# Kernel tuning notes

Measured on AMD Instinct MI355X. Metric: run time of the kernel, lower is better.

The kernel has to match this reference:

```python
import jax, jax.numpy as jnp
import numpy as np

EMB = 64
HID = 1024
SEQ = 9
BATCH = 4096


def setup_inputs() -> dict:
    key = jax.random.key(0)
    ks = jax.random.split(key, 10)
    s = lambda *sh: 1.0 / np.sqrt(sh[-1])
    return {
        "observed": jax.random.normal(ks[0], (SEQ, BATCH, 2), dtype=jnp.float32),
        "W_emb": jax.random.normal(ks[1], (EMB, 2), dtype=jnp.float32) * s(2),
        "b_emb": jnp.zeros((EMB,), dtype=jnp.float32),
        "W_ih": jax.random.normal(ks[2], (4 * HID, EMB), dtype=jnp.float32) * s(EMB),
        "b_ih": jnp.zeros((4 * HID,), dtype=jnp.float32),
        "W_hh": jax.random.normal(ks[3], (4 * HID, HID), dtype=jnp.float32) * s(HID),
        "b_hh": jnp.zeros((4 * HID,), dtype=jnp.float32),
        "W_out": jax.random.normal(ks[4], (5, HID), dtype=jnp.float32) * s(HID),
        "b_out": jnp.zeros((5,), dtype=jnp.float32),
        "n_predict": 12,
    }


def _cell(x, h, c, W_ih, b_ih, W_hh, b_hh):
    # torch.nn.LSTMCell gate math, gate order i, f, g, o
    gates = x @ W_ih.T + b_ih + h @ W_hh.T + b_hh  # [B, 4H]
    i, f, g, o = jnp.split(gates, 4, axis=-1)
    c_new = jax.nn.sigmoid(f) * c + jax.nn.sigmoid(i) * jnp.tanh(g)
    h_new = jax.nn.sigmoid(o) * jnp.tanh(c_new)
    return h_new, c_new


def reference(observed, W_emb, b_emb, W_ih, b_ih, W_hh, b_hh, W_out, b_out, n_predict):
    B = observed.shape[1]
    H = W_hh.shape[1]
    h0 = jnp.zeros((B, H), dtype=observed.dtype)
    c0 = jnp.zeros((B, H), dtype=observed.dtype)

    diffs = observed[1:] - observed[:-1]  # [SEQ-1, B, 2]

    def obs_step(carry, d):
        h, c = carry
        emb = jax.nn.relu(d @ W_emb.T + b_emb)  # [B, EMB]
        h, c = _cell(emb, h, c, W_ih, b_ih, W_hh, b_hh)
        normal = h @ W_out.T + b_out  # [B, 5]
        return (h, c), normal

    (h, c), normals_obs = jax.lax.scan(obs_step, (h0, c0), diffs)
    new_vel = normals_obs[-1][:, :2]

    def pred_step(carry, _):
        h, c, nv = carry
        emb = jax.nn.relu(jax.lax.stop_gradient(nv) @ W_emb.T + b_emb)
        h, c = _cell(emb, h, c, W_ih, b_ih, W_hh, b_hh)
        normal = h @ W_out.T + b_out
        return (h, c, normal[:, :2]), normal

    (_, _, _), normals_pred = jax.lax.scan(
        pred_step, (h, c, new_vel), None, length=n_predict - 1)

    # training-mode output: stacked raw 'normal' params, shape [SEQ-1+n_predict-1, B, 5]
    return jnp.concatenate([normals_obs, normals_pred], axis=0)
```

## Files before the change

### kernel.cpp

```cpp
#include <hip/hip_runtime.h>
#include <stdint.h>
#include <stddef.h>

#define BATCH 4096
#define HID   1024
#define EMB   64
#define KDIM  1088
#define NKT   34
#define NSTEP 19
#define NOBS  8

typedef _Float16 f16;
typedef _Float16 half8 __attribute__((ext_vector_type(8)));
typedef float    float4v __attribute__((ext_vector_type(4)));

__device__ __forceinline__ float sigm(float x) { return 1.f / (1.f + __expf(-x)); }
__device__ __forceinline__ float tanh_f(float x) { return 1.f - 2.f / (__expf(2.f * x) + 1.f); }

__device__ __forceinline__ int xf_idx(int row, int k) {
  return ((((row >> 4) * NKT + (k >> 5)) * 64) + (row & 15) + (((k >> 3) & 3) << 4)) * 8 + (k & 7);
}

__global__ void pack_kernel(const float* __restrict__ W_ih, const float* __restrict__ b_ih,
                            const float* __restrict__ W_hh, const float* __restrict__ b_hh,
                            f16* __restrict__ Wsw, float* __restrict__ bc) {
  int gid = blockIdx.x * blockDim.x + threadIdx.x;
  int j = gid & 7;
  int lane = (gid >> 3) & 63;
  int c16 = (gid >> 9) & 255;
  int kt = gid >> 17;
  int p = c16 * 16 + (lane & 15);
  int k = kt * 32 + ((lane >> 4) << 3) + j;
  int t = p >> 7, g = (p >> 5) & 3, u = p & 31;
  int orig = g * HID + t * 32 + u;
  float val = (k < EMB) ? W_ih[orig * EMB + k] : W_hh[orig * HID + (k - EMB)];
  Wsw[gid] = (f16)val;
  if (k == 0) bc[p] = b_ih[orig] + b_hh[orig];
}

__global__ void emb0_kernel(const float* __restrict__ observed,
                            const float* __restrict__ W_emb, const float* __restrict__ b_emb,
                            f16* __restrict__ Xf) {
  int gid = blockIdx.x * blockDim.x + threadIdx.x;
  int b = gid >> 6, j = gid & 63;
  const float* o0 = observed + b * 2;
  const float* o1 = o0 + BATCH * 2;
  float d0 = o1[0] - o0[0];
  float d1 = o1[1] - o0[1];
  float v = d0 * W_emb[2 * j] + d1 * W_emb[2 * j + 1] + b_emb[j];
  Xf[xf_idx(b, j)] = (f16)fmaxf(v, 0.f);
}

__global__ __launch_bounds__(256, 2)
void gemm_cell_kernel(const f16* __restrict__ Xf, const f16* __restrict__ Wsw,
                      const float* __restrict__ bc,
                      f16* __restrict__ c_ws, f16* __restrict__ Xn,
                      float* __restrict__ po_ws, const float* __restrict__ W_out,
                      const float* __restrict__ obs_next, int do_emb,
                      const float* __restrict__ W_emb, const float* __restrict__ b_emb) {
  const int tid = threadIdx.x;
  const int lane = tid & 63;
  const int w = tid >> 6;
  const int l15 = lane & 15;
  const int quad = lane >> 4;
  const int tt = blockIdx.x;
  const int mB = blockIdx.y;
  const int rt0 = mB * 16 + w * 4;

  const f16* aB = Xf + (size_t)rt0 * (NKT * 512) + lane * 8;
  const f16* bB = Wsw + (size_t)tt * 8 * 512 + lane * 8;

  float4v acc[4][8];
#pragma unroll
  for (int mi = 0; mi < 4; ++mi)
#pragma unroll
    for (int ni = 0; ni < 8; ++ni) acc[mi][ni] = (float4v){0.f, 0.f, 0.f, 0.f};

  half8 afA[4], bfA[8], afB[4], bfB[8];

#define LOADF(af, bf, kt)                                                          \
  do {                                                                             \
    _Pragma("unroll") for (int mi = 0; mi < 4; ++mi)                               \
        af[mi] = *(const half8*)(aB + mi * (NKT * 512) + (kt) * 512);              \
    _Pragma("unroll") for (int ni = 0; ni < 8; ++ni)                               \
        bf[ni] = *(const half8*)(bB + ni * 512 + (kt) * 131072);                   \
  } while (0)

#define MFMA_ALL(af, bf)                                                           \
  do {                                                                             \
    _Pragma("unroll") for (int mi = 0; mi < 4; ++mi)                               \
    _Pragma("unroll") for (int ni = 0; ni < 8; ++ni)                               \
        acc[mi][ni] =                                                              \
            __builtin_amdgcn_mfma_f32_16x16x32_f16(af[mi], bf[ni], acc[mi][ni], 0, 0, 0); \
  } while (0)

  LOADF(afA, bfA, 0);
  for (int i = 0; i < NKT / 2; ++i) {
    const int k1 = 2 * i + 1;
    LOADF(afB, bfB, k1);
    MFMA_ALL(afA, bfA);
    if (k1 + 1 < NKT) LOADF(afA, bfA, k1 + 1);
    MFMA_ALL(afB, bfB);
  }
#undef LOADF
#undef MFMA_ALL

  float bias[8];
#pragma unroll
  for (int ni = 0; ni < 8; ++ni) bias[ni] = bc[tt * 128 + ni * 16 + l15];

  float wb[2][5];
#pragma unroll
  for (int u16 = 0; u16 < 2; ++u16)
#pragma unroll
    for (int o = 0; o < 5; ++o)
      wb[u16][o] = W_out[o * HID + tt * 32 + u16 * 16 + l15];

  f16* cbase = c_ws + ((size_t)(mB * 32 + tt) * 256 + tid) * 32;
  half8 cv8[4];
#pragma unroll
  for (int q = 0; q < 4; ++q) cv8[q] = *(const half8*)(cbase + q * 8);

#pragma unroll
  for (int mi = 0; mi < 4; ++mi) {
#pragma unroll
    for (int r = 0; r < 4; ++r) {
      const int row = mB * 256 + w * 64 + mi * 16 + quad * 4 + r;
      float pa[5] = {0.f, 0.f, 0.f, 0.f, 0.f};
#pragma unroll
      for (int u16 = 0; u16 < 2; ++u16) {
        const int j = tt * 32 + u16 * 16 + l15;
        const int ce = (mi * 2 + u16) * 4 + r;
        float gi = acc[mi][u16 + 0][r] + bias[u16 + 0];
        float gf = acc[mi][u16 + 2][r] + bias[u16 + 2];
        float gg = acc[mi][u16 + 4][r] + bias[u16 + 4];
        float go = acc[mi][u16 + 6][r] + bias[u16 + 6];
        float co = (float)cv8[ce >> 3][ce & 7];
        float cn = sigm(gf) * co + sigm(gi) * tanh_f(gg);
        cv8[ce >> 3][ce & 7] = (f16)cn;
        float h = sigm(go) * tanh_f(cn);
        Xn[xf_idx(row, EMB + j)] = (f16)h;
#pragma unroll
        for (int o = 0; o < 5; ++o) pa[o] += h * wb[u16][o];
      }
#pragma unroll
      for (int o = 0; o < 5; ++o) {
        pa[o] += __shfl_xor(pa[o], 1, 64);
        pa[o] += __shfl_xor(pa[o], 2, 64);
        pa[o] += __shfl_xor(pa[o], 4, 64);
        pa[o] += __shfl_xor(pa[o], 8, 64);
      }
      if (l15 == 0) {
        float* pdst = po_ws + ((size_t)tt * BATCH + row) * 5;
#pragma unroll
        for (int o = 0; o < 5; ++o) pdst[o] = pa[o];
      }
    }
  }
#pragma unroll
  for (int q = 0; q < 4; ++q) *(half8*)(cbase + q * 8) = cv8[q];

  if (do_emb && tt == 0) {
    const int row = mB * 256 + tid;
    const float* o0 = obs_next + row * 2;
    const float* o1 = o0 + BATCH * 2;
    float d0 = o1[0] - o0[0];
    float d1 = o1[1] - o0[1];
    const int rt = row >> 4;
#pragma unroll
    for (int kt = 0; kt < 2; ++kt)
#pragma unroll
      for (int kl = 0; kl < 4; ++kl) {
        half8 hv;
#pragma unroll
        for (int e = 0; e < 8; ++e) {
          int j = kt * 32 + kl * 8 + e;
          float v = d0 * W_emb[2 * j] + d1 * W_emb[2 * j + 1] + b_emb[j];
          hv[e] = (f16)fmaxf(v, 0.f);
        }
        *(half8*)(Xn + (((rt * NKT + kt) * 64) + (row & 15) + 16 * kl) * 8) = hv;
      }
  }
}

__global__ __launch_bounds__(256)
void reduce_kernel(const float* __restrict__ po_ws, const float* __restrict__ b_out,
                   float* __restrict__ out_t, int emb_flag,
                   const float* __restrict__ W_emb, const float* __restrict__ b_emb,
                   f16* __restrict__ Xn) {
  __shared__ float s_nv[32][2];
  const int tid = threadIdx.x;
  const int r0 = blockIdx.x * 32;

  if (tid < 160) {
    const int rowl = tid / 5, o = tid - rowl * 5;
    const int row = r0 + rowl;
    float s = 0.f;
#pragma unroll
    for (int tt = 0; tt < 32; ++tt) s += po_ws[((size_t)tt * BATCH + row) * 5 + o];
    float v = s + b_out[o];
    out_t[(size_t)row * 5 + o] = v;
    if (o < 2) s_nv[rowl][o] = v;
  }
  if (emb_flag) {
    __syncthreads();
    const int rowl = tid >> 3, kt = (tid >> 2) & 1, kl = tid & 3;
    const int row = r0 + rowl;
    const float d0 = s_nv[rowl][0], d1 = s_nv[rowl][1];
    half8 hv;
#pragma unroll
    for (int e = 0; e < 8; ++e) {
      int j = kt * 32 + kl * 8 + e;
      float v = d0 * W_emb[2 * j] + d1 * W_emb[2 * j + 1] + b_emb[j];
      hv[e] = (f16)fmaxf(v, 0.f);
    }
    *(half8*)(Xn + ((((row >> 4) * NKT + kt) * 64) + (row & 15) + 16 * kl) * 8) = hv;
  }
}

extern "C" void kernel_launch(void* const* d_in, const int* in_sizes, int n_in,
                              void* d_out, int out_size, void* d_ws, size_t ws_size,
                              hipStream_t stream) {
  const float* observed = (const float*)d_in[0];
  const float* W_emb = (const float*)d_in[1];
  const float* b_emb = (const float*)d_in[2];
  const float* W_ih = (const float*)d_in[3];
  const float* b_ih = (const float*)d_in[4];
  const float* W_hh = (const float*)d_in[5];
  const float* b_hh = (const float*)d_in[6];
  const float* W_out = (const float*)d_in[7];
  const float* b_out = (const float*)d_in[8];
  float* out = (float*)d_out;

  uint8_t* ws = (uint8_t*)d_ws;
  const size_t WC_BYTES = (size_t)4096 * KDIM * sizeof(f16);
  f16* Wsw = (f16*)ws;
  float* bc = (float*)(ws + WC_BYTES);
  f16* X0 = (f16*)(ws + WC_BYTES + 16384);
  f16* X1 = (f16*)(ws + 2 * WC_BYTES + 16384);
  f16* c_ws = (f16*)(ws + 3 * WC_BYTES + 16384);
  float* po_ws = (float*)(ws + 3 * WC_BYTES + 16384 + (size_t)BATCH * HID * 2);

  pack_kernel<<<(4096 * KDIM) / 256, 256, 0, stream>>>(W_ih, b_ih, W_hh, b_hh, Wsw, bc);
  hipMemsetAsync(X0, 0, WC_BYTES, stream);
  hipMemsetAsync(c_ws, 0, (size_t)BATCH * HID * 2, stream);
  emb0_kernel<<<(BATCH * EMB) / 256, 256, 0, stream>>>(observed, W_emb, b_emb, X0);

  for (int t = 0; t < NSTEP; ++t) {
    f16* Xc = (t & 1) ? X1 : X0;
    f16* Xn = (t & 1) ? X0 : X1;
    const int do_emb = (t + 1 < NOBS) ? 1 : 0;
    dim3 grid(32, 16);
    gemm_cell_kernel<<<grid, 256, 0, stream>>>(
        Xc, Wsw, bc, c_ws, Xn, po_ws, W_out,
        observed + (size_t)(t + 1) * BATCH * 2, do_emb, W_emb, b_emb);
    const int emb_pred = (t >= 7 && t + 1 < NSTEP) ? 1 : 0;
    reduce_kernel<<<BATCH / 32, 256, 0, stream>>>(
        po_ws, b_out, out + (size_t)t * BATCH * 5, emb_pred, W_emb, b_emb, Xn);
  }
}
```

Measured before the change: 1.145 ms.

## Fuse embedding and output reduction into LSTM gemm, drop reduce kernel

Computes the ReLU embedding inside the gemm kernel as the first two K-tiles of MFMA, fed from observed diffs or the previous step's output, so the separate emb0 and reduce kernels go away. The output projection is now accumulated into a bias-prefilled output buffer with atomicAdd instead of a partial-sum workspace plus reduction pass. Step 0 skips the recurrent GEMM because h is zero, and the weight layout is changed so each tile's K slice is contiguous, with a swizzled block order for cache locality. The cost is float atomics (non-deterministic summation order) and embedding recomputation in every block.

```diff
diff --git a/kernel.cpp b/kernel.cpp
--- a/kernel.cpp
+++ b/kernel.cpp
@@ -5,10 +5,11 @@
 #define BATCH 4096
 #define HID   1024
 #define EMB   64
-#define KDIM  1088
+#define NKH   32
 #define NKT   34
 #define NSTEP 19
 #define NOBS  8
+#define WSL   139264
 
 typedef _Float16 f16;
 typedef _Float16 half8 __attribute__((ext_vector_type(8)));
@@ -16,59 +17,53 @@
 
 __device__ __forceinline__ float sigm(float x) { return 1.f / (1.f + __expf(-x)); }
 __device__ __forceinline__ float tanh_f(float x) { return 1.f - 2.f / (__expf(2.f * x) + 1.f); }
-
-__device__ __forceinline__ int xf_idx(int row, int k) {
-  return ((((row >> 4) * NKT + (k >> 5)) * 64) + (row & 15) + (((k >> 3) & 3) << 4)) * 8 + (k & 7);
-}
 
 __global__ void pack_kernel(const float* __restrict__ W_ih, const float* __restrict__ b_ih,
                             const float* __restrict__ W_hh, const float* __restrict__ b_hh,
                             f16* __restrict__ Wsw, float* __restrict__ bc) {
   int gid = blockIdx.x * blockDim.x + threadIdx.x;
-  int j = gid & 7;
-  int lane = (gid >> 3) & 63;
-  int c16 = (gid >> 9) & 255;
-  int kt = gid >> 17;
-  int p = c16 * 16 + (lane & 15);
-  int k = kt * 32 + ((lane >> 4) << 3) + j;
-  int t = p >> 7, g = (p >> 5) & 3, u = p & 31;
-  int orig = g * HID + t * 32 + u;
+  int tt = gid / WSL;
+  int rem = gid - tt * WSL;
+  int kt = rem >> 12;
+  int ni = (rem >> 9) & 7;
+  int lane = (rem >> 3) & 63;
+  int e = rem & 7;
+  int p = tt * 128 + ni * 16 + (lane & 15);
+  int g = (p >> 5) & 3;
+  int u = p & 31;
+  int orig = g * HID + tt * 32 + u;
+  int k = kt * 32 + ((lane >> 4) << 3) + e;
   float val = (k < EMB) ? W_ih[orig * EMB + k] : W_hh[orig * HID + (k - EMB)];
   Wsw[gid] = (f16)val;
   if (k == 0) bc[p] = b_ih[orig] + b_hh[orig];
 }
 
-__global__ void emb0_kernel(const float* __restrict__ observed,
-                            const float* __restrict__ W_emb, const float* __restrict__ b_emb,
-                            f16* __restrict__ Xf) {
+__global__ void outinit_kernel(float* __restrict__ out, const float* __restrict__ b_out) {
   int gid = blockIdx.x * blockDim.x + threadIdx.x;
-  int b = gid >> 6, j = gid & 63;
-  const float* o0 = observed + b * 2;
-  const float* o1 = o0 + BATCH * 2;
-  float d0 = o1[0] - o0[0];
-  float d1 = o1[1] - o0[1];
-  float v = d0 * W_emb[2 * j] + d1 * W_emb[2 * j + 1] + b_emb[j];
-  Xf[xf_idx(b, j)] = (f16)fmaxf(v, 0.f);
+  out[gid] = b_out[gid % 5];
 }
 
 __global__ __launch_bounds__(256, 2)
-void gemm_cell_kernel(const f16* __restrict__ Xf, const f16* __restrict__ Wsw,
+void gemm_cell_kernel(const f16* __restrict__ Xp, const f16* __restrict__ Wsw,
                       const float* __restrict__ bc,
                       f16* __restrict__ c_ws, f16* __restrict__ Xn,
-                      float* __restrict__ po_ws, const float* __restrict__ W_out,
-                      const float* __restrict__ obs_next, int do_emb,
-                      const float* __restrict__ W_emb, const float* __restrict__ b_emb) {
+                      float* __restrict__ out_t, const float* __restrict__ W_out,
+                      const float* __restrict__ obs_t, const float* __restrict__ outprev,
+                      int mode, const float* __restrict__ W_emb,
+                      const float* __restrict__ b_emb) {
   const int tid = threadIdx.x;
   const int lane = tid & 63;
   const int w = tid >> 6;
   const int l15 = lane & 15;
   const int quad = lane >> 4;
-  const int tt = blockIdx.x;
-  const int mB = blockIdx.y;
+  const int id = blockIdx.x;
+  const int x = id & 7, s = id >> 3;
+  const int tt = ((x >> 1) << 3) | (s & 7);
+  const int mB = ((x & 1) << 3) | (s >> 3);
   const int rt0 = mB * 16 + w * 4;
 
-  const f16* aB = Xf + (size_t)rt0 * (NKT * 512) + lane * 8;
-  const f16* bB = Wsw + (size_t)tt * 8 * 512 + lane * 8;
+  const f16* aB = Xp + (size_t)rt0 * (NKH * 512) + lane * 8;
+  const f16* bB = Wsw + (size_t)tt * WSL + lane * 8;
 
   float4v acc[4][8];
 #pragma unroll
@@ -76,16 +71,55 @@
 #pragma unroll
     for (int ni = 0; ni < 8; ++ni) acc[mi][ni] = (float4v){0.f, 0.f, 0.f, 0.f};
 
-  half8 afA[4], bfA[8], afB[4], bfB[8];
-
-#define LOADF(af, bf, kt)                                                          \
+  {
+    float d0[4], d1[4];
+#pragma unroll
+    for (int mi = 0; mi < 4; ++mi) {
+      const int row = (rt0 + mi) * 16 + l15;
+      if (mode <= 1) {
+        const float* o = obs_t + row * 2;
+        d0[mi] = o[BATCH * 2] - o[0];
+        d1[mi] = o[BATCH * 2 + 1] - o[1];
+      } else {
+        d0[mi] = outprev[(size_t)row * 5 + 0];
+        d1[mi] = outprev[(size_t)row * 5 + 1];
+      }
+    }
+#pragma unroll
+    for (int kt = 0; kt < 2; ++kt) {
+      float w0[8], w1[8], be[8];
+#pragma unroll
+      for (int e = 0; e < 8; ++e) {
+        int j = kt * 32 + quad * 8 + e;
+        w0[e] = W_emb[2 * j];
+        w1[e] = W_emb[2 * j + 1];
+        be[e] = b_emb[j];
+      }
+      half8 bf[8];
+#pragma unroll
+      for (int ni = 0; ni < 8; ++ni) bf[ni] = *(const half8*)(bB + kt * 4096 + ni * 512);
+#pragma unroll
+      for (int mi = 0; mi < 4; ++mi) {
+        half8 ae;
+#pragma unroll
+        for (int e = 0; e < 8; ++e)
+          ae[e] = (f16)fmaxf(d0[mi] * w0[e] + d1[mi] * w1[e] + be[e], 0.f);
+#pragma unroll
+        for (int ni = 0; ni < 8; ++ni)
+          acc[mi][ni] = __builtin_amdgcn_mfma_f32_16x16x32_f16(ae, bf[ni], acc[mi][ni], 0, 0, 0);
+      }
+    }
+  }
+
+  if (mode >= 1) {
+    half8 afA[4], bfA[8], afB[4], bfB[8];
+#define LOADF(af, bf, kh)                                                          \
   do {                                                                             \
     _Pragma("unroll") for (int mi = 0; mi < 4; ++mi)                               \
-        af[mi] = *(const half8*)(aB + mi * (NKT * 512) + (kt) * 512);              \
+        af[mi] = *(const half8*)(aB + mi * (NKH * 512) + (kh) * 512);              \
     _Pragma("unroll") for (int ni = 0; ni < 8; ++ni)                               \
-        bf[ni] = *(const half8*)(bB + ni * 512 + (kt) * 131072);                   \
+        bf[ni] = *(const half8*)(bB + ((kh) + 2) * 4096 + ni * 512);               \
   } while (0)
-
 #define MFMA_ALL(af, bf)                                                           \
   do {                                                                             \
     _Pragma("unroll") for (int mi = 0; mi < 4; ++mi)                               \
@@ -93,22 +127,21 @@
         acc[mi][ni] =                                                              \
             __builtin_amdgcn_mfma_f32_16x16x32_f16(af[mi], bf[ni], acc[mi][ni], 0, 0, 0); \
   } while (0)
-
-  LOADF(afA, bfA, 0);
-  for (int i = 0; i < NKT / 2; ++i) {
-    const int k1 = 2 * i + 1;
-    LOADF(afB, bfB, k1);
-    MFMA_ALL(afA, bfA);
-    if (k1 + 1 < NKT) LOADF(afA, bfA, k1 + 1);
-    MFMA_ALL(afB, bfB);
-  }
+    LOADF(afA, bfA, 0);
+    for (int i = 0; i < NKH / 2; ++i) {
+      const int k1 = 2 * i + 1;
+      LOADF(afB, bfB, k1);
+      MFMA_ALL(afA, bfA);
+      if (k1 + 1 < NKH) LOADF(afA, bfA, k1 + 1);
+      MFMA_ALL(afB, bfB);
+    }
 #undef LOADF
 #undef MFMA_ALL
+  }
 
   float bias[8];
 #pragma unroll
   for (int ni = 0; ni < 8; ++ni) bias[ni] = bc[tt * 128 + ni * 16 + l15];
-
   float wb[2][5];
 #pragma unroll
   for (int u16 = 0; u16 < 2; ++u16)
@@ -129,17 +162,17 @@
       float pa[5] = {0.f, 0.f, 0.f, 0.f, 0.f};
 #pragma unroll
       for (int u16 = 0; u16 < 2; ++u16) {
-        const int j = tt * 32 + u16 * 16 + l15;
         const int ce = (mi * 2 + u16) * 4 + r;
         float gi = acc[mi][u16 + 0][r] + bias[u16 + 0];
         float gf = acc[mi][u16 + 2][r] + bias[u16 + 2];
         float gg = acc[mi][u16 + 4][r] + bias[u16 + 4];
         float go = acc[mi][u16 + 6][r] + bias[u16 + 6];
-        float co = (float)cv8[ce >> 3][ce & 7];
+        float co = (mode == 0) ? 0.f : (float)cv8[ce >> 3][ce & 7];
         float cn = sigm(gf) * co + sigm(gi) * tanh_f(gg);
         cv8[ce >> 3][ce & 7] = (f16)cn;
         float h = sigm(go) * tanh_f(cn);
-        Xn[xf_idx(row, EMB + j)] = (f16)h;
+        Xn[(((size_t)(row >> 4) * NKH + tt) * 64 + (row & 15) + 16 * (u16 * 2 + (l15 >> 3))) * 8 +
+           (l15 & 7)] = (f16)h;
 #pragma unroll
         for (int o = 0; o < 5; ++o) pa[o] += h * wb[u16][o];
       }
@@ -151,71 +184,14 @@
         pa[o] += __shfl_xor(pa[o], 8, 64);
       }
       if (l15 == 0) {
-        float* pdst = po_ws + ((size_t)tt * BATCH + row) * 5;
-#pragma unroll
-        for (int o = 0; o < 5; ++o) pdst[o] = pa[o];
+        float* pdst = out_t + (size_t)row * 5;
+#pragma unroll
+        for (int o = 0; o < 5; ++o) atomicAdd(pdst + o, pa[o]);
       }
     }
   }
 #pragma unroll
   for (int q = 0; q < 4; ++q) *(half8*)(cbase + q * 8) = cv8[q];
-
-  if (do_emb && tt == 0) {
-    const int row = mB * 256 + tid;
-    const float* o0 = obs_next + row * 2;
-    const float* o1 = o0 + BATCH * 2;
-    float d0 = o1[0] - o0[0];
-    float d1 = o1[1] - o0[1];
-    const int rt = row >> 4;
-#pragma unroll
-    for (int kt = 0; kt < 2; ++kt)
-#pragma unroll
-      for (int kl = 0; kl < 4; ++kl) {
-        half8 hv;
-#pragma unroll
-        for (int e = 0; e < 8; ++e) {
-          int j = kt * 32 + kl * 8 + e;
-          float v = d0 * W_emb[2 * j] + d1 * W_emb[2 * j + 1] + b_emb[j];
-          hv[e] = (f16)fmaxf(v, 0.f);
-        }
-        *(half8*)(Xn + (((rt * NKT + kt) * 64) + (row & 15) + 16 * kl) * 8) = hv;
-      }
-  }
-}
-
-__global__ __launch_bounds__(256)
-void reduce_kernel(const float* __restrict__ po_ws, const float* __restrict__ b_out,
-                   float* __restrict__ out_t, int emb_flag,
-                   const float* __restrict__ W_emb, const float* __restrict__ b_emb,
-                   f16* __restrict__ Xn) {
-  __shared__ float s_nv[32][2];
-  const int tid = threadIdx.x;
-  const int r0 = blockIdx.x * 32;
-
-  if (tid < 160) {
-    const int rowl = tid / 5, o = tid - rowl * 5;
-    const int row = r0 + rowl;
-    float s = 0.f;
-#pragma unroll
-    for (int tt = 0; tt < 32; ++tt) s += po_ws[((size_t)tt * BATCH + row) * 5 + o];
-    float v = s + b_out[o];
-    out_t[(size_t)row * 5 + o] = v;
-    if (o < 2) s_nv[rowl][o] = v;
-  }
-  if (emb_flag) {
-    __syncthreads();
-    const int rowl = tid >> 3, kt = (tid >> 2) & 1, kl = tid & 3;
-    const int row = r0 + rowl;
-    const float d0 = s_nv[rowl][0], d1 = s_nv[rowl][1];
-    half8 hv;
-#pragma unroll
-    for (int e = 0; e < 8; ++e) {
-      int j = kt * 32 + kl * 8 + e;
-      float v = d0 * W_emb[2 * j] + d1 * W_emb[2 * j + 1] + b_emb[j];
-      hv[e] = (f16)fmaxf(v, 0.f);
-    }
-    *(half8*)(Xn + ((((row >> 4) * NKT + kt) * 64) + (row & 15) + 16 * kl) * 8) = hv;
-  }
 }
 
 extern "C" void kernel_launch(void* const* d_in, const int* in_sizes, int n_in,
@@ -233,29 +209,24 @@
   float* out = (float*)d_out;
 
   uint8_t* ws = (uint8_t*)d_ws;
-  const size_t WC_BYTES = (size_t)4096 * KDIM * sizeof(f16);
+  const size_t WSW_BYTES = (size_t)32 * WSL * sizeof(f16);
+  const size_t XH_BYTES = (size_t)256 * NKH * 64 * 8 * sizeof(f16);
   f16* Wsw = (f16*)ws;
-  float* bc = (float*)(ws + WC_BYTES);
-  f16* X0 = (f16*)(ws + WC_BYTES + 16384);
-  f16* X1 = (f16*)(ws + 2 * WC_BYTES + 16384);
-  f16* c_ws = (f16*)(ws + 3 * WC_BYTES + 16384);
-  float* po_ws = (float*)(ws + 3 * WC_BYTES + 16384 + (size_t)BATCH * HID * 2);
-
-  pack_kernel<<<(4096 * KDIM) / 256, 256, 0, stream>>>(W_ih, b_ih, W_hh, b_hh, Wsw, bc);
-  hipMemsetAsync(X0, 0, WC_BYTES, stream);
-  hipMemsetAsync(c_ws, 0, (size_t)BATCH * HID * 2, stream);
-  emb0_kernel<<<(BATCH * EMB) / 256, 256, 0, stream>>>(observed, W_emb, b_emb, X0);
+  float* bc = (float*)(ws + WSW_BYTES);
+  f16* X0 = (f16*)(ws + WSW_BYTES + 16384);
+  f16* X1 = (f16*)(ws + WSW_BYTES + 16384 + XH_BYTES);
+  f16* c_ws = (f16*)(ws + WSW_BYTES + 16384 + 2 * XH_BYTES);
+
+  pack_kernel<<<(32 * WSL) / 256, 256, 0, stream>>>(W_ih, b_ih, W_hh, b_hh, Wsw, bc);
+  outinit_kernel<<<(NSTEP * BATCH * 5) / 256, 256, 0, stream>>>(out, b_out);
 
   for (int t = 0; t < NSTEP; ++t) {
     f16* Xc = (t & 1) ? X1 : X0;
-    f16* Xn = (t & 1) ? X0 : X1;
-    const int do_emb = (t + 1 < NOBS) ? 1 : 0;
-    dim3 grid(32, 16);
-    gemm_cell_kernel<<<grid, 256, 0, stream>>>(
-        Xc, Wsw, bc, c_ws, Xn, po_ws, W_out,
-        observed + (size_t)(t + 1) * BATCH * 2, do_emb, W_emb, b_emb);
-    const int emb_pred = (t >= 7 && t + 1 < NSTEP) ? 1 : 0;
-    reduce_kernel<<<BATCH / 32, 256, 0, stream>>>(
-        po_ws, b_out, out + (size_t)t * BATCH * 5, emb_pred, W_emb, b_emb, Xn);
-  }
-}
+    f16* Xp = (t & 1) ? X0 : X1;
+    const int mode = (t == 0) ? 0 : (t < NOBS ? 1 : 2);
+    gemm_cell_kernel<<<512, 256, 0, stream>>>(
+        Xp, Wsw, bc, c_ws, Xc, out + (size_t)t * BATCH * 5, W_out,
+        observed + (size_t)t * BATCH * 2, out + (size_t)(t - 1) * BATCH * 5,
+        mode, W_emb, b_emb);
+  }
+}
```

Result: slower. 2.262 ms (+97.6%).
